# Kernel optimization log

Measured on AMD Instinct MI355X. Metric: run time of the kernel, lower is better.

The kernel has to match this reference:

```python
import jax, jax.numpy as jnp
import numpy as np


def setup_inputs() -> dict:
    key = jax.random.key(0)
    k1, k2 = jax.random.split(key)
    H = W = 4096
    input1 = jax.random.normal(k1, (1, 1, H, W), dtype=jnp.float32)   # moving image
    input2 = jax.random.normal(k2, (1, 2, H, W), dtype=jnp.float32)   # dense flow (dH, dW)
    return {"input1": input1, "input2": input2}


def reference(input1, input2):
    # input1: [B=1, C=1, H, W] image; input2: [B=1, 2, H, W] displacement field
    B, C, H, W = input1.shape
    f32 = jnp.float32

    # identity mesh (matches torch.linspace outer-product construction)
    h_mesh = jnp.broadcast_to(jnp.arange(H, dtype=f32)[None, :, None], (B, H, W))
    w_mesh = jnp.broadcast_to(jnp.arange(W, dtype=f32)[None, None, :], (B, H, W))

    # warped sampling coordinates, shifted by +1 for the zero-padding border
    H_up = (input2[:, 0] + h_mesh).reshape(-1) + 1.0   # [B*H*W]
    W_up = (input2[:, 1] + w_mesh).reshape(-1) + 1.0

    # zero-pad image by 1 pixel on each spatial side
    img = jnp.pad(input1, ((0, 0), (0, 0), (1, 1), (1, 1)))  # [B, C, H+2, W+2]
    Hp, Wp = H + 2, W + 2

    hf = jnp.floor(H_up).astype(jnp.int32)
    hc = hf + 1
    wf = jnp.floor(W_up).astype(jnp.int32)
    wc = wf + 1
    hf = jnp.clip(hf, 0, Hp - 1)
    hc = jnp.clip(hc, 0, Hp - 1)
    wf = jnp.clip(wf, 0, Wp - 1)
    wc = jnp.clip(wc, 0, Wp - 1)

    img_flat = img.reshape(-1)  # B = C = 1
    val_000 = img_flat[hf * Wp + wf]
    val_010 = img_flat[hc * Wp + wf]
    val_001 = img_flat[hf * Wp + wc]
    val_011 = img_flat[hc * Wp + wc]

    dH = hc.astype(f32) - H_up
    dW = wc.astype(f32) - W_up
    out = (val_000 * (dW * dH)
           + val_010 * (dW * (1.0 - dH))
           + val_001 * ((1.0 - dW) * dH)
           + val_011 * ((1.0 - dW) * (1.0 - dH)))

    # [B*H*W] -> [B, H, W, C] -> [B, C, H, W]
    return out.reshape(B, H, W, C).transpose(0, 3, 1, 2)
```

## Files before the change

kernel.cpp:

```cpp
#include <hip/hip_runtime.h>


#define IMG_H 4096
#define IMG_W 4096

__global__ __launch_bounds__(256) void warp_bilinear_kernel(
    const float* __restrict__ img,
    const float* __restrict__ flow,
    float* __restrict__ out)
{
    const int HW = IMG_H * IMG_W;
    const int lane = threadIdx.x & 63;
    const int wv   = threadIdx.x >> 6;
    const int h = blockIdx.y * 4 + wv;
    const int w = blockIdx.x * 64 + lane;
    const int idx = h * IMG_W + w;

    const float fh = flow[idx];
    const float fw = flow[HW + idx];

    float Hu = (fh + (float)h) + 1.0f;
    float Wu = (fw + (float)w) + 1.0f;

    int hf = (int)floorf(Hu);
    int wf = (int)floorf(Wu);
    int hc = hf + 1;
    int wc = wf + 1;

    int hfc = min(max(hf, 0), IMG_H + 1);
    int hcc = min(max(hc, 0), IMG_H + 1);
    int wfc = min(max(wf, 0), IMG_W + 1);
    int wcc = min(max(wc, 0), IMG_W + 1);

    float dH = (float)hcc - Hu;
    float dW = (float)wcc - Wu;

    bool hf_in = (hfc >= 1) && (hfc <= IMG_H);
    bool hc_in = (hcc >= 1) && (hcc <= IMG_H);
    bool wf_in = (wfc >= 1) && (wfc <= IMG_W);
    bool wc_in = (wcc >= 1) && (wcc <= IMG_W);

    long rowf = (long)(hfc - 1) * IMG_W;
    long rowc = (long)(hcc - 1) * IMG_W;

    float v00 = (hf_in && wf_in) ? img[rowf + (wfc - 1)] : 0.0f;
    float v10 = (hc_in && wf_in) ? img[rowc + (wfc - 1)] : 0.0f;
    float v01 = (hf_in && wc_in) ? img[rowf + (wcc - 1)] : 0.0f;
    float v11 = (hc_in && wc_in) ? img[rowc + (wcc - 1)] : 0.0f;

    float res = v00 * (dW * dH)
              + v10 * (dW * (1.0f - dH))
              + v01 * ((1.0f - dW) * dH)
              + v11 * ((1.0f - dW) * (1.0f - dH));

    out[idx] = res;
}

extern "C" void kernel_launch(void* const* d_in, const int* in_sizes, int n_in,
                              void* d_out, int out_size, void* d_ws, size_t ws_size,
                              hipStream_t stream) {
    const float* img  = (const float*)d_in[0];
    const float* flow = (const float*)d_in[1];
    float* out = (float*)d_out;

    dim3 grid(IMG_W / 64, IMG_H / 4);
    dim3 block(256);
    warp_bilinear_kernel<<<grid, block, 0, stream>>>(img, flow, out);
}
```

Measured before the change: 265.5 us.

## Stage image tile with halo in LDS for bilinear gathers

Each block loads a 64x16 output tile's image neighborhood plus an 8-pixel margin into shared memory using coalesced float4 loads, then performs the four bilinear gathers from LDS. Samples whose displacement falls outside the margin fall back to global loads. This removes scattered global gather traffic at the cost of extra halo reads, a block-wide barrier, and a divergent slow path for large displacements.

```diff
diff --git a/kernel.cpp b/kernel.cpp
--- a/kernel.cpp
+++ b/kernel.cpp
@@ -3,57 +3,111 @@
 
 #define IMG_H 4096
 #define IMG_W 4096
+#define TILE_W 64
+#define TILE_H 16
+#define MARGIN 8
+#define SROWS (TILE_H + 2*MARGIN)
+#define SCOLS (TILE_W + 2*MARGIN)
+#define SSTRIDE 84
 
 __global__ __launch_bounds__(256) void warp_bilinear_kernel(
     const float* __restrict__ img,
     const float* __restrict__ flow,
     float* __restrict__ out)
 {
-    const int HW = IMG_H * IMG_W;
-    const int lane = threadIdx.x & 63;
-    const int wv   = threadIdx.x >> 6;
-    const int h = blockIdx.y * 4 + wv;
-    const int w = blockIdx.x * 64 + lane;
-    const int idx = h * IMG_W + w;
+    __shared__ float tile[SROWS * SSTRIDE];
 
-    const float fh = flow[idx];
-    const float fw = flow[HW + idx];
+    const int tid  = threadIdx.x;
+    const int h0   = blockIdx.y * TILE_H;
+    const int w0   = blockIdx.x * TILE_W;
+    const int row0 = h0 - MARGIN;
+    const int col0 = w0 - MARGIN;
+    const int HW   = IMG_H * IMG_W;
 
-    float Hu = (fh + (float)h) + 1.0f;
-    float Wu = (fw + (float)w) + 1.0f;
+    const bool interior = (row0 >= 0) && (row0 + SROWS <= IMG_H) &&
+                          (col0 >= 0) && (col0 + SCOLS <= IMG_W);
 
-    int hf = (int)floorf(Hu);
-    int wf = (int)floorf(Wu);
-    int hc = hf + 1;
-    int wc = wf + 1;
+    if (interior) {
+        #pragma unroll
+        for (int base = 0; base < 3; ++base) {
+            int t = base * 256 + tid;
+            if (t < SROWS * 20) {
+                int r = t / 20, c4 = t % 20;
+                const float4 v = *reinterpret_cast<const float4*>(
+                    img + (long)(row0 + r) * IMG_W + col0 + c4 * 4);
+                *reinterpret_cast<float4*>(&tile[r * SSTRIDE + c4 * 4]) = v;
+            }
+        }
+    } else {
+        for (int t = tid; t < SROWS * SCOLS; t += 256) {
+            int r = t / SCOLS, c = t % SCOLS;
+            int gr = row0 + r, gc = col0 + c;
+            float v = (gr >= 0 && gr < IMG_H && gc >= 0 && gc < IMG_W)
+                      ? img[(long)gr * IMG_W + gc] : 0.0f;
+            tile[r * SSTRIDE + c] = v;
+        }
+    }
+    __syncthreads();
 
-    int hfc = min(max(hf, 0), IMG_H + 1);
-    int hcc = min(max(hc, 0), IMG_H + 1);
-    int wfc = min(max(wf, 0), IMG_W + 1);
-    int wcc = min(max(wc, 0), IMG_W + 1);
+    const int lane = tid & 63;
+    const int wv   = tid >> 6;
+    const int w    = w0 + lane;
 
-    float dH = (float)hcc - Hu;
-    float dW = (float)wcc - Wu;
+    #pragma unroll
+    for (int k = 0; k < 4; ++k) {
+        const int h   = h0 + wv * 4 + k;
+        const int idx = h * IMG_W + w;
 
-    bool hf_in = (hfc >= 1) && (hfc <= IMG_H);
-    bool hc_in = (hcc >= 1) && (hcc <= IMG_H);
-    bool wf_in = (wfc >= 1) && (wfc <= IMG_W);
-    bool wc_in = (wcc >= 1) && (wcc <= IMG_W);
+        const float fh = flow[idx];
+        const float fw = flow[HW + idx];
 
-    long rowf = (long)(hfc - 1) * IMG_W;
-    long rowc = (long)(hcc - 1) * IMG_W;
+        float Hu = (fh + (float)h) + 1.0f;
+        float Wu = (fw + (float)w) + 1.0f;
 
-    float v00 = (hf_in && wf_in) ? img[rowf + (wfc - 1)] : 0.0f;
-    float v10 = (hc_in && wf_in) ? img[rowc + (wfc - 1)] : 0.0f;
-    float v01 = (hf_in && wc_in) ? img[rowf + (wcc - 1)] : 0.0f;
-    float v11 = (hc_in && wc_in) ? img[rowc + (wcc - 1)] : 0.0f;
+        int hf = (int)floorf(Hu);
+        int wf = (int)floorf(Wu);
+        int hc = hf + 1;
+        int wc = wf + 1;
 
-    float res = v00 * (dW * dH)
-              + v10 * (dW * (1.0f - dH))
-              + v01 * ((1.0f - dW) * dH)
-              + v11 * ((1.0f - dW) * (1.0f - dH));
+        int hfc = min(max(hf, 0), IMG_H + 1);
+        int hcc = min(max(hc, 0), IMG_H + 1);
+        int wfc = min(max(wf, 0), IMG_W + 1);
+        int wcc = min(max(wc, 0), IMG_W + 1);
 
-    out[idx] = res;
+        float dH = (float)hcc - Hu;
+        float dW = (float)wcc - Wu;
+
+        int trf = (hfc - 1) - row0;
+        int trc = (hcc - 1) - row0;
+        int tcf = (wfc - 1) - col0;
+        int tcc = (wcc - 1) - col0;
+
+        float v00, v10, v01, v11;
+        bool in_tile = ((unsigned)trf < SROWS) && ((unsigned)trc < SROWS) &&
+                       ((unsigned)tcf < SCOLS) && ((unsigned)tcc < SCOLS);
+        if (__builtin_expect(in_tile, 1)) {
+            v00 = tile[trf * SSTRIDE + tcf];
+            v10 = tile[trc * SSTRIDE + tcf];
+            v01 = tile[trf * SSTRIDE + tcc];
+            v11 = tile[trc * SSTRIDE + tcc];
+        } else {
+            bool hf_in = (hfc >= 1) && (hfc <= IMG_H);
+            bool hc_in = (hcc >= 1) && (hcc <= IMG_H);
+            bool wf_in = (wfc >= 1) && (wfc <= IMG_W);
+            bool wc_in = (wcc >= 1) && (wcc <= IMG_W);
+            long rowf = (long)(hfc - 1) * IMG_W;
+            long rowc = (long)(hcc - 1) * IMG_W;
+            v00 = (hf_in && wf_in) ? img[rowf + (wfc - 1)] : 0.0f;
+            v10 = (hc_in && wf_in) ? img[rowc + (wfc - 1)] : 0.0f;
+            v01 = (hf_in && wc_in) ? img[rowf + (wcc - 1)] : 0.0f;
+            v11 = (hc_in && wc_in) ? img[rowc + (wcc - 1)] : 0.0f;
+        }
+
+        out[idx] = v00 * (dW * dH)
+                 + v10 * (dW * (1.0f - dH))
+                 + v01 * ((1.0f - dW) * dH)
+                 + v11 * ((1.0f - dW) * (1.0f - dH));
+    }
 }
 
 extern "C" void kernel_launch(void* const* d_in, const int* in_sizes, int n_in,
@@ -63,7 +117,7 @@
     const float* flow = (const float*)d_in[1];
     float* out = (float*)d_out;
 
-    dim3 grid(IMG_W / 64, IMG_H / 4);
+    dim3 grid(IMG_W / TILE_W, IMG_H / TILE_H);
     dim3 block(256);
     warp_bilinear_kernel<<<grid, block, 0, stream>>>(img, flow, out);
 }
```

Result: no change. 270.3 us (+1.8%).

## Process four rows per thread with branchless clamped gathers and nontemporal flow/output access

Applied to the files above, without the earlier changes.

Each thread now handles four output pixels spaced four rows apart. All flow loads are issued first, then all 16 image gathers, so more memory requests are in flight per thread. Out-of-bounds taps are handled by clamping the address and zeroing the weight rather than predicating the load, which lets every gather issue unconditionally. Flow reads and output writes use nontemporal hints to keep streaming data from displacing image lines in cache. The cost is higher register pressure and a grid four times smaller.

```diff
diff --git a/kernel.cpp b/kernel.cpp
--- a/kernel.cpp
+++ b/kernel.cpp
@@ -9,51 +9,88 @@
     const float* __restrict__ flow,
     float* __restrict__ out)
 {
-    const int HW = IMG_H * IMG_W;
+    const int HW   = IMG_H * IMG_W;
     const int lane = threadIdx.x & 63;
     const int wv   = threadIdx.x >> 6;
-    const int h = blockIdx.y * 4 + wv;
-    const int w = blockIdx.x * 64 + lane;
-    const int idx = h * IMG_W + w;
+    const int w    = blockIdx.x * 64 + lane;
+    const int h0   = blockIdx.y * 16 + wv;
 
-    const float fh = flow[idx];
-    const float fw = flow[HW + idx];
+    int   idx[4];
+    float fh[4], fw[4];
 
-    float Hu = (fh + (float)h) + 1.0f;
-    float Wu = (fw + (float)w) + 1.0f;
+    #pragma unroll
+    for (int k = 0; k < 4; ++k)
+        idx[k] = (h0 + 4 * k) * IMG_W + w;
 
-    int hf = (int)floorf(Hu);
-    int wf = (int)floorf(Wu);
-    int hc = hf + 1;
-    int wc = wf + 1;
+    #pragma unroll
+    for (int k = 0; k < 4; ++k)
+        fh[k] = __builtin_nontemporal_load(flow + idx[k]);
+    #pragma unroll
+    for (int k = 0; k < 4; ++k)
+        fw[k] = __builtin_nontemporal_load(flow + HW + idx[k]);
 
-    int hfc = min(max(hf, 0), IMG_H + 1);
-    int hcc = min(max(hc, 0), IMG_H + 1);
-    int wfc = min(max(wf, 0), IMG_W + 1);
-    int wcc = min(max(wc, 0), IMG_W + 1);
+    int   o00[4], o10[4], o01[4], o11[4];
+    float w00[4], w10[4], w01[4], w11[4];
 
-    float dH = (float)hcc - Hu;
-    float dW = (float)wcc - Wu;
+    #pragma unroll
+    for (int k = 0; k < 4; ++k) {
+        const int h = h0 + 4 * k;
+        float Hu = (fh[k] + (float)h) + 1.0f;
+        float Wu = (fw[k] + (float)w) + 1.0f;
 
-    bool hf_in = (hfc >= 1) && (hfc <= IMG_H);
-    bool hc_in = (hcc >= 1) && (hcc <= IMG_H);
-    bool wf_in = (wfc >= 1) && (wfc <= IMG_W);
-    bool wc_in = (wcc >= 1) && (wcc <= IMG_W);
+        int hf = (int)floorf(Hu);
+        int wf = (int)floorf(Wu);
+        int hc = hf + 1;
+        int wc = wf + 1;
 
-    long rowf = (long)(hfc - 1) * IMG_W;
-    long rowc = (long)(hcc - 1) * IMG_W;
+        int hfc = min(max(hf, 0), IMG_H + 1);
+        int hcc = min(max(hc, 0), IMG_H + 1);
+        int wfc = min(max(wf, 0), IMG_W + 1);
+        int wcc = min(max(wc, 0), IMG_W + 1);
 
-    float v00 = (hf_in && wf_in) ? img[rowf + (wfc - 1)] : 0.0f;
-    float v10 = (hc_in && wf_in) ? img[rowc + (wfc - 1)] : 0.0f;
-    float v01 = (hf_in && wc_in) ? img[rowf + (wcc - 1)] : 0.0f;
-    float v11 = (hc_in && wc_in) ? img[rowc + (wcc - 1)] : 0.0f;
+        float dH = (float)hcc - Hu;
+        float dW = (float)wcc - Wu;
 
-    float res = v00 * (dW * dH)
-              + v10 * (dW * (1.0f - dH))
-              + v01 * ((1.0f - dW) * dH)
-              + v11 * ((1.0f - dW) * (1.0f - dH));
+        int rf = hfc - 1, rc = hcc - 1, cf = wfc - 1, cc = wcc - 1;
+        bool rf_in = (unsigned)rf < IMG_H;
+        bool rc_in = (unsigned)rc < IMG_H;
+        bool cf_in = (unsigned)cf < IMG_W;
+        bool cc_in = (unsigned)cc < IMG_W;
+        int rf_cl = min(max(rf, 0), IMG_H - 1);
+        int rc_cl = min(max(rc, 0), IMG_H - 1);
+        int cf_cl = min(max(cf, 0), IMG_W - 1);
+        int cc_cl = min(max(cc, 0), IMG_W - 1);
 
-    out[idx] = res;
+        o00[k] = (rf_cl << 12) + cf_cl;
+        o10[k] = (rc_cl << 12) + cf_cl;
+        o01[k] = (rf_cl << 12) + cc_cl;
+        o11[k] = (rc_cl << 12) + cc_cl;
+
+        float A = dW * dH;
+        float B = dW * (1.0f - dH);
+        float C = (1.0f - dW) * dH;
+        float D = (1.0f - dW) * (1.0f - dH);
+        w00[k] = (rf_in && cf_in) ? A : 0.0f;
+        w10[k] = (rc_in && cf_in) ? B : 0.0f;
+        w01[k] = (rf_in && cc_in) ? C : 0.0f;
+        w11[k] = (rc_in && cc_in) ? D : 0.0f;
+    }
+
+    float v00[4], v10[4], v01[4], v11[4];
+    #pragma unroll
+    for (int k = 0; k < 4; ++k) {
+        v00[k] = img[o00[k]];
+        v10[k] = img[o10[k]];
+        v01[k] = img[o01[k]];
+        v11[k] = img[o11[k]];
+    }
+
+    #pragma unroll
+    for (int k = 0; k < 4; ++k) {
+        float res = v00[k] * w00[k] + v10[k] * w10[k]
+                  + v01[k] * w01[k] + v11[k] * w11[k];
+        __builtin_nontemporal_store(res, out + idx[k]);
+    }
 }
 
 extern "C" void kernel_launch(void* const* d_in, const int* in_sizes, int n_in,
@@ -63,7 +100,7 @@
     const float* flow = (const float*)d_in[1];
     float* out = (float*)d_out;
 
-    dim3 grid(IMG_W / 64, IMG_H / 4);
+    dim3 grid(IMG_W / 64, IMG_H / 16);
     dim3 block(256);
     warp_bilinear_kernel<<<grid, block, 0, stream>>>(img, flow, out);
 }
```

After: 254.2 us. -4.2%, faster.
